# Kernel optimization log

Hardware: AMD Instinct MI355X
Metric: run time of the kernel (lower is better)

Reference implementation:

```python
import jax, jax.numpy as jnp
import numpy as np

B, N, D = 8, 4096, 2048
DL = 64
NCLS = 2


def setup_inputs() -> dict:
    key = jax.random.key(0)
    k_x, k_tn, k_v, k_w, k_fw, k_fb = jax.random.split(key, 6)
    x = jax.random.normal(k_x, (B, N, D), dtype=jnp.float32)
    # valid patch counts in [1, N] so no bag is fully masked
    true_num = jax.random.randint(k_tn, (B,), 1, N + 1, dtype=jnp.int32)
    std1 = 1.0 / np.sqrt(DL * D)
    V = jax.random.uniform(k_v, (D, DL), minval=-std1, maxval=std1, dtype=jnp.float32)
    std2 = 1.0 / np.sqrt(DL)
    W = jax.random.uniform(k_w, (DL, 1), minval=-std2, maxval=std2, dtype=jnp.float32)
    lim = 1.0 / np.sqrt(D)  # nn.Linear default init
    fc_w = jax.random.uniform(k_fw, (NCLS, D), minval=-lim, maxval=lim, dtype=jnp.float32)
    fc_b = jax.random.uniform(k_fb, (NCLS,), minval=-lim, maxval=lim, dtype=jnp.float32)
    return {"x": x, "true_num": true_num, "V": V, "W": W, "fc_w": fc_w, "fc_b": fc_b}


def reference(x, true_num, V, W, fc_w, fc_b):
    # MILAtten: attention scores over N patches
    x_ = jnp.tanh(jnp.einsum("bnd,dl->bnl", x, V))            # B x N x dl
    dis = jnp.einsum("bnl,lo->bn", x_, W) / np.sqrt(DL)        # B x N
    mask = jnp.arange(x.shape[1])[None, :] < true_num[:, None]  # B x N valid mask
    dis = jnp.where(mask, dis, jnp.float32(-1e20))
    soft_assign = jax.nn.softmax(dis, axis=1)                  # B x N
    feat_fusion = jnp.einsum("bn,bnd->bd", soft_assign, x)     # B x D
    # eval mode: dropout is identity
    logits = feat_fusion @ fc_w.T + fc_b                       # B x class_num
    cls_probs = jax.nn.softmax(logits, axis=1)
    return (cls_probs, soft_assign)
```

## Files before the change

### kernel.cpp

```cpp
#include <hip/hip_runtime.h>
#include <math.h>

#define BB 8
#define NN 4096
#define DD 2048

typedef __attribute__((ext_vector_type(8))) short bf16x8;
typedef __attribute__((ext_vector_type(4))) float f32x4;

__device__ __forceinline__ short f2bf(float f) {
    unsigned int u = __float_as_uint(f);
    unsigned int r = (u + 0x7fffu + ((u >> 16) & 1u)) >> 16;
    return (short)r;
}
__device__ __forceinline__ float bf2f(short s) {
    return __uint_as_float(((unsigned int)(unsigned short)s) << 16);
}

__global__ __launch_bounds__(256) void k_pack_v(const float* __restrict__ V,
                                                short* __restrict__ Vp,
                                                float* __restrict__ qblk) {
    int e = blockIdx.x * 256 + threadIdx.x;
    if (e < 4096) qblk[e] = 0.f;
    int lane = e & 63, kc = (e >> 6) & 63, w = e >> 12;
    int q = lane >> 4, mm = lane & 15;
    int kb = kc * 32 + q * 8, l = w * 16 + mm;
    bf16x8 o;
    #pragma unroll
    for (int j = 0; j < 8; j++) o[j] = f2bf(V[(size_t)(kb + j) * 64 + l]);
    *(bf16x8*)(Vp + (size_t)e * 8) = o;
}

__global__ __launch_bounds__(256, 2) void k_fused(
        const float* __restrict__ x, const int* __restrict__ tn_p,
        const short* __restrict__ Vp, const float* __restrict__ W,
        const float* __restrict__ fc_w,
        float* __restrict__ dis, float* __restrict__ mblk,
        float* __restrict__ lblk, float* __restrict__ qblk,
        float* __restrict__ dpart, float* __restrict__ erow_g) {
    __shared__ short Xs[16 * 2048];

    const int tid = threadIdx.x;
    const int blk = blockIdx.x;
    const int b  = blk >> 8;
    const int n0 = (blk & 255) << 4;
    const int tn = tn_p[b];
    if (n0 >= tn) return;

    const float4* xsrc = (const float4*)(x + ((size_t)(b * NN + n0)) * DD);
    #pragma unroll 8
    for (int i = 0; i < 32; i++) {
        int e = tid + (i << 8);
        int row = e >> 9, f4 = e & 511;
        float4 v = xsrc[(size_t)row * 512 + f4];
        int c = f4 >> 1, h = f4 & 1;
        int sc = c ^ (row & 7);
        short4 s;
        s.x = f2bf(v.x); s.y = f2bf(v.y); s.z = f2bf(v.z); s.w = f2bf(v.w);
        *(short4*)&Xs[row * 2048 + sc * 8 + h * 4] = s;
    }
    __syncthreads();

    const int lane = tid & 63, w = tid >> 6;
    const int mm = lane & 15, q = lane >> 4;
    const short* vp = Vp + (size_t)w * 32768 + lane * 8;
    const int arow = mm * 2048;
    const int msw = mm & 7;
    f32x4 acc = {0.f, 0.f, 0.f, 0.f};
    #pragma unroll 4
    for (int kc = 0; kc < 64; kc++) {
        bf16x8 a  = *(const bf16x8*)&Xs[arow + (((kc * 4 + q) ^ msw) << 3)];
        bf16x8 bv = *(const bf16x8*)(vp + kc * 512);
        acc = __builtin_amdgcn_mfma_f32_16x16x32_bf16(a, bv, acc, 0, 0, 0);
    }

    const float wl = W[w * 16 + mm];
    float* dpb = dpart + blk * 64;
    #pragma unroll
    for (int r = 0; r < 4; r++) {
        float p = tanhf(acc[r]) * wl;
        p += __shfl_xor(p, 1, 64);
        p += __shfl_xor(p, 2, 64);
        p += __shfl_xor(p, 4, 64);
        p += __shfl_xor(p, 8, 64);
        if (mm == 0) dpb[w * 16 + q * 4 + r] = p;
    }
    __syncthreads();

    if (w == 0) {
        float d = (dpb[mm] + dpb[16 + mm] + dpb[32 + mm] + dpb[48 + mm]) * 0.125f;
        int n = n0 + mm;
        if (n >= tn) d = -1e20f;
        if (lane < 16) dis[b * NN + n] = d;
        float mx = d;
        mx = fmaxf(mx, __shfl_xor(mx, 1, 64));
        mx = fmaxf(mx, __shfl_xor(mx, 2, 64));
        mx = fmaxf(mx, __shfl_xor(mx, 4, 64));
        mx = fmaxf(mx, __shfl_xor(mx, 8, 64));
        float e = expf(d - mx);
        float ls = e;
        ls += __shfl_xor(ls, 1, 64);
        ls += __shfl_xor(ls, 2, 64);
        ls += __shfl_xor(ls, 4, 64);
        ls += __shfl_xor(ls, 8, 64);
        if (lane < 16) erow_g[blk * 16 + lane] = e;
        if (lane == 0) { mblk[blk] = mx; lblk[blk] = ls; }
    }
    __syncthreads();

    float er[16];
    const float* eg = erow_g + blk * 16;
    #pragma unroll
    for (int r = 0; r < 16; r++) er[r] = eg[r];

    float facc[8];
    #pragma unroll
    for (int u = 0; u < 8; u++) facc[u] = 0.f;
    #pragma unroll
    for (int r = 0; r < 16; r++) {
        bf16x8 sv = *(const bf16x8*)&Xs[r * 2048 + ((tid ^ (r & 7)) << 3)];
        float e = er[r];
        #pragma unroll
        for (int u = 0; u < 8; u++) facc[u] = fmaf(e, bf2f(sv[u]), facc[u]);
    }
    const float4* w0p = (const float4*)fc_w + tid * 2;
    const float4* w1p = (const float4*)(fc_w + DD) + tid * 2;
    float4 wa = w0p[0], wb = w0p[1], wc = w1p[0], wd = w1p[1];
    float q0 = facc[0] * wa.x + facc[1] * wa.y + facc[2] * wa.z + facc[3] * wa.w +
               facc[4] * wb.x + facc[5] * wb.y + facc[6] * wb.z + facc[7] * wb.w;
    float q1 = facc[0] * wc.x + facc[1] * wc.y + facc[2] * wc.z + facc[3] * wc.w +
               facc[4] * wd.x + facc[5] * wd.y + facc[6] * wd.z + facc[7] * wd.w;
    #pragma unroll
    for (int o = 32; o >= 1; o >>= 1) {
        q0 += __shfl_xor(q0, o, 64);
        q1 += __shfl_xor(q1, o, 64);
    }
    if (lane == 0) {
        atomicAdd(&qblk[blk * 2 + 0], q0);
        atomicAdd(&qblk[blk * 2 + 1], q1);
    }
}

__global__ __launch_bounds__(256) void k_final(
        const float* __restrict__ dis, const int* __restrict__ tn_p,
        const float* __restrict__ mblk, const float* __restrict__ lblk,
        const float* __restrict__ qblk, const float* __restrict__ fc_b,
        float* __restrict__ soft, float* __restrict__ cls) {
    __shared__ float red[4];
    __shared__ float r3[3][4];
    __shared__ float bc;
    const int b = blockIdx.x, t = threadIdx.x;
    const int tn = tn_p[b];
    const int nvb = (tn + 15) >> 4;

    float mt = (t < nvb) ? mblk[b * 256 + t] : -3.4e38f;
    float mx = mt;
    #pragma unroll
    for (int o = 32; o >= 1; o >>= 1) mx = fmaxf(mx, __shfl_xor(mx, o, 64));
    if ((t & 63) == 0) red[t >> 6] = mx;
    __syncthreads();
    if (t == 0) bc = fmaxf(fmaxf(red[0], red[1]), fmaxf(red[2], red[3]));
    __syncthreads();
    const float M = bc;

    float sc = (t < nvb) ? expf(mt - M) : 0.f;
    float ls = (t < nvb) ? sc * lblk[b * 256 + t] : 0.f;
    float l0 = 0.f, l1 = 0.f;
    if (t < nvb) {
        l0 = sc * qblk[(b * 256 + t) * 2 + 0];
        l1 = sc * qblk[(b * 256 + t) * 2 + 1];
    }
    #pragma unroll
    for (int o = 32; o >= 1; o >>= 1) {
        ls += __shfl_xor(ls, o, 64);
        l0 += __shfl_xor(l0, o, 64);
        l1 += __shfl_xor(l1, o, 64);
    }
    if ((t & 63) == 0) {
        r3[0][t >> 6] = ls; r3[1][t >> 6] = l0; r3[2][t >> 6] = l1;
    }
    __syncthreads();
    if (t == 0) {
        float L  = r3[0][0] + r3[0][1] + r3[0][2] + r3[0][3];
        float Q0 = r3[1][0] + r3[1][1] + r3[1][2] + r3[1][3];
        float Q1 = r3[2][0] + r3[2][1] + r3[2][2] + r3[2][3];
        float L0 = Q0 / L + fc_b[0];
        float L1 = Q1 / L + fc_b[1];
        float mm2 = fmaxf(L0, L1);
        float e0 = expf(L0 - mm2), e1 = expf(L1 - mm2);
        float inv = 1.f / (e0 + e1);
        cls[b * 2 + 0] = e0 * inv;
        cls[b * 2 + 1] = e1 * inv;
        bc = 1.f / L;
    }
    __syncthreads();
    const float iL = bc;

    const float4* dv4 = (const float4*)(dis + (size_t)b * NN);
    float4* sv4 = (float4*)(soft + (size_t)b * NN);
    for (int i = t; i < NN / 4; i += 256) {
        int n = i * 4;
        float4 dv = dv4[i];
        float4 o;
        o.x = (n + 0 < tn) ? expf(dv.x - M) * iL : 0.f;
        o.y = (n + 1 < tn) ? expf(dv.y - M) * iL : 0.f;
        o.z = (n + 2 < tn) ? expf(dv.z - M) * iL : 0.f;
        o.w = (n + 3 < tn) ? expf(dv.w - M) * iL : 0.f;
        sv4[i] = o;
    }
}

extern "C" void kernel_launch(void* const* d_in, const int* in_sizes, int n_in,
                              void* d_out, int out_size, void* d_ws, size_t ws_size,
                              hipStream_t stream) {
    (void)in_sizes; (void)n_in; (void)out_size; (void)ws_size;
    const float* x        = (const float*)d_in[0];
    const int*   true_num = (const int*)d_in[1];
    const float* V        = (const float*)d_in[2];
    const float* W        = (const float*)d_in[3];
    const float* fc_w     = (const float*)d_in[4];
    const float* fc_b     = (const float*)d_in[5];

    float* out  = (float*)d_out;
    float* cls  = out;
    float* soft = out + BB * 2;

    float* dis   = (float*)d_ws;
    float* mblk  = dis + (size_t)BB * NN;
    float* lblk  = mblk + 2048;
    float* qblk  = lblk + 2048;
    float* dpart = qblk + 4096;
    float* erow  = dpart + (size_t)2048 * 64;
    short* Vp    = (short*)(erow + (size_t)2048 * 16);

    k_pack_v<<<64, 256, 0, stream>>>(V, Vp, qblk);
    k_fused<<<2048, 256, 0, stream>>>(x, true_num, Vp, W, fc_w,
                                      dis, mblk, lblk, qblk, dpart, erow);
    k_final<<<BB, 256, 0, stream>>>(dis, true_num, mblk, lblk, qblk, fc_b,
                                    soft, cls);
}
```

Measured before the change: 359.2 us.

## Prefetch V fragments, nontemporal x loads, drop atomics, split final kernel

Loads x with nontemporal loads, issues the V-fragment and W/fc_w loads before the barrier, and double-buffers V fragments across the MFMA loop. The per-block atomics into qblk are replaced by plain per-wave stores, so the zeroing in the pack kernel goes away. The final kernel now runs 32 blocks instead of 8, with each block writing one quarter of a batch's softmax row. The extra live registers for prefetch and fc_w may reduce occupancy, and every final block repeats the full reduction over block maxima.

```diff
diff --git a/kernel.cpp b/kernel.cpp
--- a/kernel.cpp
+++ b/kernel.cpp
@@ -18,10 +18,8 @@
 }
 
 __global__ __launch_bounds__(256) void k_pack_v(const float* __restrict__ V,
-                                                short* __restrict__ Vp,
-                                                float* __restrict__ qblk) {
+                                                short* __restrict__ Vp) {
     int e = blockIdx.x * 256 + threadIdx.x;
-    if (e < 4096) qblk[e] = 0.f;
     int lane = e & 63, kc = (e >> 6) & 63, w = e >> 12;
     int q = lane >> 4, mm = lane & 15;
     int kb = kc * 32 + q * 8, l = w * 16 + mm;
@@ -47,34 +45,54 @@
     const int tn = tn_p[b];
     if (n0 >= tn) return;
 
-    const float4* xsrc = (const float4*)(x + ((size_t)(b * NN + n0)) * DD);
+    const int lane = tid & 63, w = tid >> 6;
+    const int mm = lane & 15, q = lane >> 4;
+
+    const f32x4* xsrc = (const f32x4*)(x + ((size_t)(b * NN + n0)) * DD);
     #pragma unroll 8
     for (int i = 0; i < 32; i++) {
         int e = tid + (i << 8);
         int row = e >> 9, f4 = e & 511;
-        float4 v = xsrc[(size_t)row * 512 + f4];
+        f32x4 v = __builtin_nontemporal_load(&xsrc[(size_t)row * 512 + f4]);
         int c = f4 >> 1, h = f4 & 1;
         int sc = c ^ (row & 7);
         short4 s;
         s.x = f2bf(v.x); s.y = f2bf(v.y); s.z = f2bf(v.z); s.w = f2bf(v.w);
         *(short4*)&Xs[row * 2048 + sc * 8 + h * 4] = s;
     }
-    __syncthreads();
-
-    const int lane = tid & 63, w = tid >> 6;
-    const int mm = lane & 15, q = lane >> 4;
-    const short* vp = Vp + (size_t)w * 32768 + lane * 8;
+
+    const bf16x8* vpv = (const bf16x8*)Vp + ((size_t)w << 12) + lane;
+    bf16x8 bvr[4];
+    #pragma unroll
+    for (int j = 0; j < 4; j++) bvr[j] = vpv[j << 6];
+    const float wl = W[w * 16 + mm];
+
+    __syncthreads();
+
     const int arow = mm * 2048;
     const int msw = mm & 7;
     f32x4 acc = {0.f, 0.f, 0.f, 0.f};
-    #pragma unroll 4
-    for (int kc = 0; kc < 64; kc++) {
-        bf16x8 a  = *(const bf16x8*)&Xs[arow + (((kc * 4 + q) ^ msw) << 3)];
-        bf16x8 bv = *(const bf16x8*)(vp + kc * 512);
-        acc = __builtin_amdgcn_mfma_f32_16x16x32_bf16(a, bv, acc, 0, 0, 0);
-    }
-
-    const float wl = W[w * 16 + mm];
+    #pragma unroll
+    for (int kc = 0; kc < 64; kc += 4) {
+        bf16x8 cur0 = bvr[0], cur1 = bvr[1], cur2 = bvr[2], cur3 = bvr[3];
+        if (kc + 4 < 64) {
+            #pragma unroll
+            for (int j = 0; j < 4; j++) bvr[j] = vpv[(kc + 4 + j) << 6];
+        }
+        bf16x8 a0 = *(const bf16x8*)&Xs[arow + ((((kc + 0) * 4 + q) ^ msw) << 3)];
+        acc = __builtin_amdgcn_mfma_f32_16x16x32_bf16(a0, cur0, acc, 0, 0, 0);
+        bf16x8 a1 = *(const bf16x8*)&Xs[arow + ((((kc + 1) * 4 + q) ^ msw) << 3)];
+        acc = __builtin_amdgcn_mfma_f32_16x16x32_bf16(a1, cur1, acc, 0, 0, 0);
+        bf16x8 a2 = *(const bf16x8*)&Xs[arow + ((((kc + 2) * 4 + q) ^ msw) << 3)];
+        acc = __builtin_amdgcn_mfma_f32_16x16x32_bf16(a2, cur2, acc, 0, 0, 0);
+        bf16x8 a3 = *(const bf16x8*)&Xs[arow + ((((kc + 3) * 4 + q) ^ msw) << 3)];
+        acc = __builtin_amdgcn_mfma_f32_16x16x32_bf16(a3, cur3, acc, 0, 0, 0);
+    }
+
+    const float4* w0p = (const float4*)fc_w + tid * 2;
+    const float4* w1p = (const float4*)(fc_w + DD) + tid * 2;
+    float4 wa = w0p[0], wb = w0p[1], wc = w1p[0], wd = w1p[1];
+
     float* dpb = dpart + blk * 64;
     #pragma unroll
     for (int r = 0; r < 4; r++) {
@@ -123,9 +141,6 @@
         #pragma unroll
         for (int u = 0; u < 8; u++) facc[u] = fmaf(e, bf2f(sv[u]), facc[u]);
     }
-    const float4* w0p = (const float4*)fc_w + tid * 2;
-    const float4* w1p = (const float4*)(fc_w + DD) + tid * 2;
-    float4 wa = w0p[0], wb = w0p[1], wc = w1p[0], wd = w1p[1];
     float q0 = facc[0] * wa.x + facc[1] * wa.y + facc[2] * wa.z + facc[3] * wa.w +
                facc[4] * wb.x + facc[5] * wb.y + facc[6] * wb.z + facc[7] * wb.w;
     float q1 = facc[0] * wc.x + facc[1] * wc.y + facc[2] * wc.z + facc[3] * wc.w +
@@ -136,8 +151,8 @@
         q1 += __shfl_xor(q1, o, 64);
     }
     if (lane == 0) {
-        atomicAdd(&qblk[blk * 2 + 0], q0);
-        atomicAdd(&qblk[blk * 2 + 1], q1);
+        qblk[blk * 8 + w * 2 + 0] = q0;
+        qblk[blk * 8 + w * 2 + 1] = q1;
     }
 }
 
@@ -149,7 +164,7 @@
     __shared__ float red[4];
     __shared__ float r3[3][4];
     __shared__ float bc;
-    const int b = blockIdx.x, t = threadIdx.x;
+    const int b = blockIdx.x >> 2, s = blockIdx.x & 3, t = threadIdx.x;
     const int tn = tn_p[b];
     const int nvb = (tn + 15) >> 4;
 
@@ -167,8 +182,9 @@
     float ls = (t < nvb) ? sc * lblk[b * 256 + t] : 0.f;
     float l0 = 0.f, l1 = 0.f;
     if (t < nvb) {
-        l0 = sc * qblk[(b * 256 + t) * 2 + 0];
-        l1 = sc * qblk[(b * 256 + t) * 2 + 1];
+        const float* qp = qblk + (size_t)(b * 256 + t) * 8;
+        l0 = sc * (qp[0] + qp[2] + qp[4] + qp[6]);
+        l1 = sc * (qp[1] + qp[3] + qp[5] + qp[7]);
     }
     #pragma unroll
     for (int o = 32; o >= 1; o >>= 1) {
@@ -182,32 +198,31 @@
     __syncthreads();
     if (t == 0) {
         float L  = r3[0][0] + r3[0][1] + r3[0][2] + r3[0][3];
-        float Q0 = r3[1][0] + r3[1][1] + r3[1][2] + r3[1][3];
-        float Q1 = r3[2][0] + r3[2][1] + r3[2][2] + r3[2][3];
-        float L0 = Q0 / L + fc_b[0];
-        float L1 = Q1 / L + fc_b[1];
-        float mm2 = fmaxf(L0, L1);
-        float e0 = expf(L0 - mm2), e1 = expf(L1 - mm2);
-        float inv = 1.f / (e0 + e1);
-        cls[b * 2 + 0] = e0 * inv;
-        cls[b * 2 + 1] = e1 * inv;
         bc = 1.f / L;
+        if (s == 0) {
+            float Q0 = r3[1][0] + r3[1][1] + r3[1][2] + r3[1][3];
+            float Q1 = r3[2][0] + r3[2][1] + r3[2][2] + r3[2][3];
+            float L0 = Q0 / L + fc_b[0];
+            float L1 = Q1 / L + fc_b[1];
+            float mm2 = fmaxf(L0, L1);
+            float e0 = expf(L0 - mm2), e1 = expf(L1 - mm2);
+            float inv = 1.f / (e0 + e1);
+            cls[b * 2 + 0] = e0 * inv;
+            cls[b * 2 + 1] = e1 * inv;
+        }
     }
     __syncthreads();
     const float iL = bc;
 
-    const float4* dv4 = (const float4*)(dis + (size_t)b * NN);
-    float4* sv4 = (float4*)(soft + (size_t)b * NN);
-    for (int i = t; i < NN / 4; i += 256) {
-        int n = i * 4;
-        float4 dv = dv4[i];
-        float4 o;
-        o.x = (n + 0 < tn) ? expf(dv.x - M) * iL : 0.f;
-        o.y = (n + 1 < tn) ? expf(dv.y - M) * iL : 0.f;
-        o.z = (n + 2 < tn) ? expf(dv.z - M) * iL : 0.f;
-        o.w = (n + 3 < tn) ? expf(dv.w - M) * iL : 0.f;
-        sv4[i] = o;
-    }
+    const int i = s * 256 + t;
+    const int n = i * 4;
+    float4 dv = ((const float4*)(dis + (size_t)b * NN))[i];
+    float4 o;
+    o.x = (n + 0 < tn) ? expf(dv.x - M) * iL : 0.f;
+    o.y = (n + 1 < tn) ? expf(dv.y - M) * iL : 0.f;
+    o.z = (n + 2 < tn) ? expf(dv.z - M) * iL : 0.f;
+    o.w = (n + 3 < tn) ? expf(dv.w - M) * iL : 0.f;
+    ((float4*)(soft + (size_t)b * NN))[i] = o;
 }
 
 extern "C" void kernel_launch(void* const* d_in, const int* in_sizes, int n_in,
@@ -229,13 +244,13 @@
     float* mblk  = dis + (size_t)BB * NN;
     float* lblk  = mblk + 2048;
     float* qblk  = lblk + 2048;
-    float* dpart = qblk + 4096;
+    float* dpart = qblk + (size_t)2048 * 8;
     float* erow  = dpart + (size_t)2048 * 64;
     short* Vp    = (short*)(erow + (size_t)2048 * 16);
 
-    k_pack_v<<<64, 256, 0, stream>>>(V, Vp, qblk);
+    k_pack_v<<<64, 256, 0, stream>>>(V, Vp);
     k_fused<<<2048, 256, 0, stream>>>(x, true_num, Vp, W, fc_w,
                                       dis, mblk, lblk, qblk, dpart, erow);
-    k_final<<<BB, 256, 0, stream>>>(dis, true_num, mblk, lblk, qblk, fc_b,
+    k_final<<<32, 256, 0, stream>>>(dis, true_num, mblk, lblk, qblk, fc_b,
                                     soft, cls);
 }
```

After: 343.2 us. 1.05x faster.
